# Kernel tuning notes

Hardware: AMD Instinct MI355X
Metric: run time of the kernel (lower is better)

The kernel has to match this reference:

```python
import jax, jax.numpy as jnp
import numpy as np

H = 32          # query heads
KVH = 8         # kv heads (GQA)
D = 128         # head dim
GROUP = 128     # quantization group size along K
THETA = 10000.0 # RoPE base


def dequant_fp4(codes, scales):
    """FP4 E2M1-style dequant: w = (code - 8) * 0.5 * per-group scale.
    codes: [K, N] int32 in [0,16); scales: [K//GROUP, N] float32."""
    K, N = codes.shape
    g = K // GROUP
    w = (codes.astype(jnp.float32) - 8.0) * 0.5
    return (w.reshape(g, GROUP, N) * scales[:, None, :]).reshape(K, N)


def apply_rope(x, pos):
    """x: [B, S, h, D]; rotate-half RoPE."""
    half = D // 2
    inv_freq = 1.0 / (THETA ** (jnp.arange(half, dtype=jnp.float32) / half))
    ang = pos.astype(jnp.float32)[:, None] * inv_freq[None, :]  # [S, half]
    cos = jnp.cos(ang)[None, :, None, :]
    sin = jnp.sin(ang)[None, :, None, :]
    x1, x2 = x[..., :half], x[..., half:]
    return jnp.concatenate([x1 * cos - x2 * sin, x2 * cos + x1 * sin], axis=-1)


def setup_inputs() -> dict:
    key = jax.random.key(0)
    ks = jax.random.split(key, 9)
    B, S, HID = 1, 2048, H * D
    KV = KVH * D
    x = jax.random.normal(ks[0], (B, S, HID), dtype=jnp.float32)
    q_codes = jax.random.randint(ks[1], (HID, HID), 0, 16, dtype=jnp.int32)
    k_codes = jax.random.randint(ks[2], (HID, KV), 0, 16, dtype=jnp.int32)
    v_codes = jax.random.randint(ks[3], (HID, KV), 0, 16, dtype=jnp.int32)
    o_codes = jax.random.randint(ks[4], (HID, HID), 0, 16, dtype=jnp.int32)
    g = HID // GROUP
    mk = lambda k, n: jax.random.uniform(k, (g, n), dtype=jnp.float32) * 0.02 + 1e-3
    q_scales = mk(ks[5], HID)
    k_scales = mk(ks[6], KV)
    v_scales = mk(ks[7], KV)
    o_scales = mk(ks[8], HID)
    return {"x": x, "q_codes": q_codes, "k_codes": k_codes, "v_codes": v_codes,
            "o_codes": o_codes, "q_scales": q_scales, "k_scales": k_scales,
            "v_scales": v_scales, "o_scales": o_scales}


def reference(x, q_codes, k_codes, v_codes, o_codes,
              q_scales, k_scales, v_scales, o_scales):
    B, S, _ = x.shape
    Wq = dequant_fp4(q_codes, q_scales)  # [HID, HID]
    Wk = dequant_fp4(k_codes, k_scales)  # [HID, KVH*D]
    Wv = dequant_fp4(v_codes, v_scales)
    Wo = dequant_fp4(o_codes, o_scales)

    q = (x @ Wq).reshape(B, S, H, D)
    k = (x @ Wk).reshape(B, S, KVH, D)
    v = (x @ Wv).reshape(B, S, KVH, D)

    pos = jnp.arange(S)
    q = apply_rope(q, pos)
    k = apply_rope(k, pos)

    # GQA: expand kv heads to query heads (this is what reading the shared
    # KV cache per query-head group computes)
    rep = H // KVH
    k = jnp.repeat(k, rep, axis=2)  # [B, S, H, D]
    v = jnp.repeat(v, rep, axis=2)

    scale = 1.0 / jnp.sqrt(jnp.float32(D))
    scores = jnp.einsum('bqhd,bkhd->bhqk', q, k) * scale  # [B, H, S, S]
    causal = jnp.tril(jnp.ones((S, S), dtype=bool))
    scores = jnp.where(causal[None, None], scores, jnp.float32(-1e30))
    probs = jax.nn.softmax(scores, axis=-1)
    attn = jnp.einsum('bhqk,bkhd->bqhd', probs, v).reshape(B, S, H * D)
    return attn @ Wo
```

## Files before the change

### kernel.cpp

```cpp
#include <hip/hip_runtime.h>

typedef unsigned short u16;
typedef __attribute__((ext_vector_type(4))) float f32x4;
typedef __attribute__((ext_vector_type(4))) unsigned short u16x4;
typedef __attribute__((ext_vector_type(8))) short bf16x8;

#define S_LEN 2048
#define NH 32
#define NKVH 8
#define DHEAD 128
#define HID 4096
#define KVW 1024
#define QKVW 6144

__device__ __forceinline__ u16 f2bf(float f) {
  unsigned u = __float_as_uint(f);
  u = u + 0x7fffu + ((u >> 16) & 1u);
  return (u16)(u >> 16);
}
__device__ __forceinline__ float bf2f(u16 h) {
  return __uint_as_float(((unsigned)h) << 16);
}
__device__ __forceinline__ void async16(void* lds, const void* g) {
  __builtin_amdgcn_global_load_lds((const __attribute__((address_space(1))) void*)g,
                                   (__attribute__((address_space(3))) void*)lds, 16, 0, 0);
}
__device__ __forceinline__ f32x4 mfma16(bf16x8 a, bf16x8 b, f32x4 c) {
  return __builtin_amdgcn_mfma_f32_16x16x32_bf16(a, b, c, 0, 0, 0);
}
__device__ __forceinline__ unsigned cvtpk(float a, float b) {
  unsigned r;
  asm("v_cvt_pk_bf16_f32 %0, %1, %2" : "=v"(r) : "v"(a), "v"(b));
  return r;
}

__global__ __launch_bounds__(256) void f2bf4_kernel(const float* __restrict__ in,
                                                    u16* __restrict__ out) {
  size_t i = ((size_t)blockIdx.x * 256 + threadIdx.x) * 4;
  f32x4 v = *(const f32x4*)(in + i);
  u16x4 o;
  o.x = f2bf(v.x); o.y = f2bf(v.y); o.z = f2bf(v.z); o.w = f2bf(v.w);
  *(u16x4*)(out + i) = o;
}

__global__ __launch_bounds__(256) void dequant_t_kernel(const int* __restrict__ codes,
                                                        const float* __restrict__ scales,
                                                        u16* __restrict__ Wt,
                                                        int K, int N) {
  __shared__ float tile[32][33];
  const int tx = threadIdx.x & 31, ty = threadIdx.x >> 5;
  const int k0 = blockIdx.x * 32, n0 = blockIdx.y * 32;
  const float sc = scales[(size_t)(k0 >> 7) * N + n0 + tx];
#pragma unroll
  for (int i = 0; i < 4; ++i) {
    int k = k0 + ty + i * 8;
    int c = codes[(size_t)k * N + n0 + tx];
    tile[ty + i * 8][tx] = ((float)c - 8.0f) * 0.5f * sc;
  }
  __syncthreads();
#pragma unroll
  for (int i = 0; i < 4; ++i) {
    int n = n0 + ty + i * 8;
    Wt[(size_t)n * K + k0 + tx] = f2bf(tile[tx][ty + i * 8]);
  }
}

template <int NI, int OUTF32>
__global__ __launch_bounds__(512, 2) void gemm_w(const u16* __restrict__ A, int lda,
                                                 const u16* __restrict__ Bt, int ldb,
                                                 void* __restrict__ Cv, int ldc, int K) {
  constexpr int BN = NI * 32;
  constexpr int NB = NI / 2;
  constexpr int BSLOT = BN * 128;
  extern __shared__ char lds[];
  char* Bbase = lds + 65536;
  const int tid = threadIdx.x, w = tid >> 6, lane = tid & 63;
  const int lo = lane & 15, hi = lane >> 4;
  const int wm = w >> 1, wn = w & 1;
  const int id = blockIdx.x;
  const int g = id & 7, r = id >> 3;
  const int bm = r >> 2, bn = g * 4 + (r & 3);
  const int m0 = bm * 256, n0 = bn * BN;

  const int srow = tid >> 3, schunk = (tid & 7) ^ (srow & 7);
  const char* Ab = (const char*)(A + (size_t)(m0 + srow) * lda) + schunk * 16;
  const char* Bb = (const char*)(Bt + (size_t)(n0 + srow) * ldb) + schunk * 16;

  f32x4 acc[4][NI];
#pragma unroll
  for (int i = 0; i < 4; ++i)
#pragma unroll
    for (int j = 0; j < NI; ++j) acc[i][j] = (f32x4){0.f, 0.f, 0.f, 0.f};

  auto stageA = [&](int buf, int k1) {
#pragma unroll
    for (int u = 0; u < 2; ++u) {
      char* dst = lds + buf * 32768 + u * 8192 + w * 1024;
      async16(dst, Ab + ((size_t)(u * 64) * lda + k1) * 2);
      async16(dst + 16384, Ab + ((size_t)(u * 64 + 128) * lda + k1) * 2);
    }
  };
  auto stageB = [&](int slot, int k1) {
#pragma unroll
    for (int j = 0; j < NB; ++j)
      async16(Bbase + slot * BSLOT + j * 8192 + w * 1024,
              Bb + ((size_t)(j * 64) * ldb + k1) * 2);
  };

  const int xm = (lo & 7) << 4;
  const int aro = (wm >> 1) * 16384 + (wm & 1) * 8192 + lo * 128;
  int bofs[NI];
#pragma unroll
  for (int ni = 0; ni < NI; ++ni) {
    int n = wn * (NI * 16) + ni * 16 + lo;
    bofs[ni] = (n >> 6) * 8192 + (n & 63) * 128;
  }

  auto ldfrags = [&](const char* As, const char* Bs, int kk, bf16x8* Afo, bf16x8* Bfo) {
    const int ck = (kk * 64 + hi * 16) ^ xm;
#pragma unroll
    for (int i = 0; i < 4; ++i) Afo[i] = *(const bf16x8*)(As + aro + i * 2048 + ck);
#pragma unroll
    for (int ni = 0; ni < NI; ++ni) Bfo[ni] = *(const bf16x8*)(Bs + bofs[ni] + ck);
  };

  stageA(0, 0);
  stageB(0, 0);
  stageB(1, 64);
  asm volatile("s_waitcnt vmcnt(%0)" ::"i"(NB) : "memory");
  __builtin_amdgcn_s_barrier();

  bf16x8 Afc[4], Bfc[NI], Afn[4], Bfn[NI];
  ldfrags(lds, Bbase, 0, Afc, Bfc);

  const int KT = K >> 6;
  int ab = 0, bb = 0;
  for (int t = 0; t < KT; ++t) {
    const char* As = lds + ab * 32768;
    const char* Bs = Bbase + bb * BSLOT;
    const bool m1 = t + 1 < KT, m2 = t + 2 < KT;
    int bs2 = bb + 2; if (bs2 >= 3) bs2 -= 3;
    int bn1 = bb + 1; if (bn1 >= 3) bn1 -= 3;
    if (m1) stageA(ab ^ 1, (t + 1) << 6);
    ldfrags(As, Bs, 1, Afn, Bfn);
    __builtin_amdgcn_sched_barrier(0);
    __builtin_amdgcn_s_setprio(1);
#pragma unroll
    for (int i = 0; i < 4; ++i)
#pragma unroll
      for (int ni = 0; ni < NI; ++ni)
        acc[i][ni] = mfma16(Afc[i], Bfc[ni], acc[i][ni]);
    __builtin_amdgcn_s_setprio(0);
    if (m2) stageB(bs2, (t + 2) << 6);
    __builtin_amdgcn_s_setprio(1);
#pragma unroll
    for (int i = 0; i < 4; ++i)
#pragma unroll
      for (int ni = 0; ni < NI; ++ni)
        acc[i][ni] = mfma16(Afn[i], Bfn[ni], acc[i][ni]);
    __builtin_amdgcn_s_setprio(0);
    if (m1) {
      if (m2) asm volatile("s_waitcnt vmcnt(%0)" ::"i"(NB) : "memory");
      else    asm volatile("s_waitcnt vmcnt(0)" ::: "memory");
      __builtin_amdgcn_s_barrier();
      ldfrags(lds + (ab ^ 1) * 32768, Bbase + bn1 * BSLOT, 0, Afc, Bfc);
      __builtin_amdgcn_sched_barrier(0);
    }
    ab ^= 1;
    if (++bb == 3) bb = 0;
  }
#pragma unroll
  for (int mi = 0; mi < 4; ++mi)
#pragma unroll
    for (int ni = 0; ni < NI; ++ni) {
      size_t row = (size_t)(m0 + wm * 64 + mi * 16 + hi * 4);
      size_t col = (size_t)(n0 + wn * (NI * 16) + ni * 16 + lo);
#pragma unroll
      for (int rr = 0; rr < 4; ++rr) {
        size_t idx = (row + rr) * ldc + col;
        if (OUTF32) ((float*)Cv)[idx] = acc[mi][ni][rr];
        else ((u16*)Cv)[idx] = f2bf(acc[mi][ni][rr]);
      }
    }
}

__global__ void rope_tab_kernel(float* __restrict__ ctab, float* __restrict__ stab) {
  int s = blockIdx.x, d = threadIdx.x;
  float inv = exp2f(-(float)d * 0.2076205059304601f);
  float ang = (float)s * inv;
  ctab[s * 64 + d] = cosf(ang);
  stab[s * 64 + d] = sinf(ang);
}

__global__ __launch_bounds__(256) void rope_kernel(u16* __restrict__ qkv,
                                                   const float* __restrict__ ctab,
                                                   const float* __restrict__ stab) {
  int s = blockIdx.x;
  int head = blockIdx.y * 4 + (threadIdx.x >> 6);
  int d = threadIdx.x & 63;
  int col = head < NH ? head * DHEAD + d : HID + (head - NH) * DHEAD + d;
  size_t base = (size_t)s * QKVW + col;
  float c = ctab[s * 64 + d], sn = stab[s * 64 + d];
  float x1 = bf2f(qkv[base]);
  float x2 = bf2f(qkv[base + 64]);
  qkv[base] = f2bf(x1 * c - x2 * sn);
  qkv[base + 64] = f2bf(x2 * c + x1 * sn);
}

__global__ __launch_bounds__(256) void vtrans_kernel(const u16* __restrict__ qkv,
                                                     u16* __restrict__ Vt) {
  __shared__ u16 tile[32][33];
  const int tx = threadIdx.x & 31, ty = threadIdx.x >> 5;
  const int s0 = blockIdx.x * 32, c0 = blockIdx.y * 32;
#pragma unroll
  for (int i = 0; i < 4; ++i)
    tile[ty + i * 8][tx] = qkv[(size_t)(s0 + ty + i * 8) * QKVW + (HID + KVW) + c0 + tx];
  __syncthreads();
#pragma unroll
  for (int i = 0; i < 4; ++i)
    Vt[(size_t)(c0 + ty + i * 8) * S_LEN + s0 + tx] = tile[tx][ty + i * 8];
}

__global__ __launch_bounds__(256) void attn_kernel(const u16* __restrict__ qkv,
                                                   const u16* __restrict__ Vt,
                                                   u16* __restrict__ attnO) {
  __shared__ alignas(16) u16 Ks[2][64 * 128];
  __shared__ alignas(16) u16 Vs[2][128 * 64];
  __shared__ alignas(16) unsigned Ps32[4][16][44];
  const int tid = threadIdx.x, w = tid >> 6, lane = tid & 63;
  const int lo = lane & 15, hi = lane >> 4;
  const int bx = blockIdx.x, h = blockIdx.y, kvh = h >> 2;
  const u16* Kbase = qkv + HID + kvh * DHEAD;
  const u16* Vbase = Vt + (size_t)kvh * DHEAD * S_LEN;
  const int krow = w * 4 + hi;
  const int kscn = lo;
  const int vrow = w * 8 + (lane >> 3);
  const int vscn = lane & 7;

#pragma unroll 1
  for (int pass = 0; pass < 2; ++pass) {
    const int qb = pass == 0 ? (31 - bx) : bx;
    const int qrow0 = qb * 64 + w * 16;
    bf16x8 qf[4];
    {
      const u16* qp = qkv + (size_t)(qrow0 + lo) * QKVW + h * DHEAD;
      const float qs = 0.08838834764831845f * 1.4426950408889634f;
#pragma unroll
      for (int dc = 0; dc < 4; ++dc) {
        bf16x8 v = *(const bf16x8*)(qp + dc * 32 + hi * 8);
#pragma unroll
        for (int j = 0; j < 8; ++j) v[j] = (short)f2bf(bf2f((u16)v[j]) * qs);
        qf[dc] = v;
      }
    }
    f32x4 oacc[8];
#pragma unroll
    for (int i = 0; i < 8; ++i) oacc[i] = (f32x4){0.f, 0.f, 0.f, 0.f};
    float m_run = -1e30f, l_run = 0.f;

    const int nt = qb + 1;
#pragma unroll
    for (int i = 0; i < 4; ++i) {
      int kr = i * 16 + krow;
      async16((char*)&Ks[0][0] + (i * 16 + w * 4) * 256,
              (const char*)(Kbase + (size_t)kr * QKVW + (kscn ^ (kr & 7)) * 8));
      int vr = i * 32 + vrow;
      async16((char*)&Vs[0][0] + (i * 32 + w * 8) * 128,
              (const char*)(Vbase + (size_t)vr * S_LEN + (vscn ^ (vr & 7)) * 8));
    }
    __syncthreads();
    for (int kt = 0; kt < nt; ++kt) {
      const int cur = kt & 1;
      if (kt + 1 < nt) {
#pragma unroll
        for (int i = 0; i < 4; ++i) {
          int kr = i * 16 + krow;
          async16((char*)&Ks[cur ^ 1][0] + (i * 16 + w * 4) * 256,
                  (const char*)(Kbase + (size_t)((kt + 1) * 64 + kr) * QKVW + (kscn ^ (kr & 7)) * 8));
          int vr = i * 32 + vrow;
          async16((char*)&Vs[cur ^ 1][0] + (i * 32 + w * 8) * 128,
                  (const char*)(Vbase + (size_t)vr * S_LEN + (kt + 1) * 64 + (vscn ^ (vr & 7)) * 8));
        }
      }
      f32x4 st[4];
#pragma unroll
      for (int t = 0; t < 4; ++t) st[t] = (f32x4){0.f, 0.f, 0.f, 0.f};
#pragma unroll
      for (int t = 0; t < 4; ++t) {
        int kq = t * 16 + lo;
#pragma unroll
        for (int dc = 0; dc < 4; ++dc) {
          bf16x8 kf = *(const bf16x8*)((const char*)&Ks[cur][0] + kq * 256 +
                                       (((dc << 2) + hi) ^ (kq & 7)) * 16);
          st[t] = mfma16(kf, qf[dc], st[t]);
        }
      }
      if (kt == qb) {
#pragma unroll
        for (int t = 0; t < 4; ++t)
#pragma unroll
          for (int r = 0; r < 4; ++r) {
            int kposl = t * 16 + 4 * hi + r;
            st[t][r] = (kposl <= w * 16 + lo) ? st[t][r] : -1e30f;
          }
      }
      float mloc = st[0][0];
#pragma unroll
      for (int t = 0; t < 4; ++t)
#pragma unroll
        for (int r = 0; r < 4; ++r) mloc = fmaxf(mloc, st[t][r]);
      mloc = fmaxf(mloc, __shfl_xor(mloc, 16, 64));
      mloc = fmaxf(mloc, __shfl_xor(mloc, 32, 64));
      if (!__all(mloc - m_run <= 8.0f)) {
        float mn = fmaxf(m_run, mloc);
        float alpha = exp2f(m_run - mn);
        m_run = mn;
        l_run *= alpha;
#pragma unroll
        for (int dt = 0; dt < 8; ++dt)
#pragma unroll
          for (int r = 0; r < 4; ++r) oacc[dt][r] *= alpha;
      }
      float psum = 0.f;
#pragma unroll
      for (int t = 0; t < 4; ++t)
#pragma unroll
        for (int r = 0; r < 4; ++r) {
          float p = exp2f(st[t][r] - m_run);
          st[t][r] = p;
          psum += p;
        }
      psum += __shfl_xor(psum, 16, 64);
      psum += __shfl_xor(psum, 32, 64);
      l_run += psum;
#pragma unroll
      for (int t = 0; t < 4; ++t)
#pragma unroll
        for (int rp = 0; rp < 2; ++rp)
          Ps32[w][lo][8 * t + 2 * hi + rp] = cvtpk(st[t][2 * rp], st[t][2 * rp + 1]);
      bf16x8 pf[2];
#pragma unroll
      for (int kc = 0; kc < 2; ++kc) pf[kc] = *(const bf16x8*)&Ps32[w][lo][kc * 16 + hi * 4];
#pragma unroll
      for (int dt = 0; dt < 8; ++dt) {
        int d = dt * 16 + lo;
#pragma unroll
        for (int kc = 0; kc < 2; ++kc) {
          bf16x8 vf = *(const bf16x8*)((const char*)&Vs[cur][0] + d * 128 +
                                       (((kc << 2) + hi) ^ (d & 7)) * 16);
          oacc[dt] = mfma16(vf, pf[kc], oacc[dt]);
        }
      }
      __syncthreads();
    }
    float linv = 1.0f / l_run;
    u16* op = attnO + (size_t)(qrow0 + lo) * HID + h * DHEAD;
#pragma unroll
    for (int dt = 0; dt < 8; ++dt) {
      u16x4 o4;
#pragma unroll
      for (int r = 0; r < 4; ++r) o4[r] = f2bf(oacc[dt][r] * linv);
      *(u16x4*)(op + dt * 16 + 4 * hi) = o4;
    }
  }
}

extern "C" void kernel_launch(void* const* d_in, const int* in_sizes, int n_in,
                              void* d_out, int out_size, void* d_ws, size_t ws_size,
                              hipStream_t stream) {
  const float* x = (const float*)d_in[0];
  const int* qc = (const int*)d_in[1];
  const int* kc = (const int*)d_in[2];
  const int* vc = (const int*)d_in[3];
  const int* oc = (const int*)d_in[4];
  const float* qs = (const float*)d_in[5];
  const float* ks = (const float*)d_in[6];
  const float* vs = (const float*)d_in[7];
  const float* os = (const float*)d_in[8];
  float* out = (float*)d_out;
  char* ws = (char*)d_ws;

  u16* xb    = (u16*)(ws);
  u16* qkv   = (u16*)(ws + 16777216);
  u16* attnb = (u16*)(ws + 41943040);
  u16* Vt    = (u16*)(ws + 58720256);
  u16* Wbig  = (u16*)(ws + 62914560);
  float* ctab = (float*)Vt;
  float* stab = (float*)(ws + 58720256 + 524288);

  f2bf4_kernel<<<8192, 256, 0, stream>>>(x, xb);
  dequant_t_kernel<<<dim3(128, 128), 256, 0, stream>>>(qc, qs, Wbig, HID, HID);
  dequant_t_kernel<<<dim3(128, 32), 256, 0, stream>>>(kc, ks, Wbig + (size_t)HID * HID, HID, KVW);
  dequant_t_kernel<<<dim3(128, 32), 256, 0, stream>>>(vc, vs, Wbig + (size_t)(HID + KVW) * HID, HID, KVW);
  rope_tab_kernel<<<2048, 64, 0, stream>>>(ctab, stab);
  gemm_w<6, 0><<<256, 512, 139264, stream>>>(xb, HID, Wbig, HID, qkv, QKVW, HID);
  rope_kernel<<<dim3(S_LEN, (NH + NKVH) / 4), 256, 0, stream>>>(qkv, ctab, stab);
  vtrans_kernel<<<dim3(64, 32), 256, 0, stream>>>(qkv, Vt);
  attn_kernel<<<dim3(16, 32), 256, 0, stream>>>(qkv, Vt, attnb);
  dequant_t_kernel<<<dim3(128, 128), 256, 0, stream>>>(oc, os, Wbig, HID, HID);
  gemm_w<4, 1><<<256, 512, 114688, stream>>>(attnb, HID, Wbig, HID, out, HID, HID);
}
```

Measured before the change: 322.7 us.

## Load K/V fragments directly from global into registers, drop LDS staging

```diff
diff --git a/kernel.cpp b/kernel.cpp
--- a/kernel.cpp
+++ b/kernel.cpp
@@ -221,21 +221,15 @@
     Vt[(size_t)(c0 + ty + i * 8) * S_LEN + s0 + tx] = tile[tx][ty + i * 8];
 }
 
-__global__ __launch_bounds__(256) void attn_kernel(const u16* __restrict__ qkv,
-                                                   const u16* __restrict__ Vt,
-                                                   u16* __restrict__ attnO) {
-  __shared__ alignas(16) u16 Ks[2][64 * 128];
-  __shared__ alignas(16) u16 Vs[2][128 * 64];
+__global__ __launch_bounds__(256, 3) void attn_kernel(const u16* __restrict__ qkv,
+                                                      const u16* __restrict__ Vt,
+                                                      u16* __restrict__ attnO) {
   __shared__ alignas(16) unsigned Ps32[4][16][44];
   const int tid = threadIdx.x, w = tid >> 6, lane = tid & 63;
   const int lo = lane & 15, hi = lane >> 4;
   const int bx = blockIdx.x, h = blockIdx.y, kvh = h >> 2;
-  const u16* Kbase = qkv + HID + kvh * DHEAD;
-  const u16* Vbase = Vt + (size_t)kvh * DHEAD * S_LEN;
-  const int krow = w * 4 + hi;
-  const int kscn = lo;
-  const int vrow = w * 8 + (lane >> 3);
-  const int vscn = lane & 7;
+  const u16* Kl = qkv + HID + kvh * DHEAD + (size_t)lo * QKVW + hi * 8;
+  const u16* Vl = Vt + (size_t)kvh * DHEAD * S_LEN + (size_t)lo * S_LEN + hi * 8;
 
 #pragma unroll 1
   for (int pass = 0; pass < 2; ++pass) {
@@ -259,42 +253,31 @@
     float m_run = -1e30f, l_run = 0.f;
 
     const int nt = qb + 1;
-#pragma unroll
-    for (int i = 0; i < 4; ++i) {
-      int kr = i * 16 + krow;
-      async16((char*)&Ks[0][0] + (i * 16 + w * 4) * 256,
-              (const char*)(Kbase + (size_t)kr * QKVW + (kscn ^ (kr & 7)) * 8));
-      int vr = i * 32 + vrow;
-      async16((char*)&Vs[0][0] + (i * 32 + w * 8) * 128,
-              (const char*)(Vbase + (size_t)vr * S_LEN + (vscn ^ (vr & 7)) * 8));
-    }
-    __syncthreads();
     for (int kt = 0; kt < nt; ++kt) {
-      const int cur = kt & 1;
-      if (kt + 1 < nt) {
-#pragma unroll
-        for (int i = 0; i < 4; ++i) {
-          int kr = i * 16 + krow;
-          async16((char*)&Ks[cur ^ 1][0] + (i * 16 + w * 4) * 256,
-                  (const char*)(Kbase + (size_t)((kt + 1) * 64 + kr) * QKVW + (kscn ^ (kr & 7)) * 8));
-          int vr = i * 32 + vrow;
-          async16((char*)&Vs[cur ^ 1][0] + (i * 32 + w * 8) * 128,
-                  (const char*)(Vbase + (size_t)vr * S_LEN + (kt + 1) * 64 + (vscn ^ (vr & 7)) * 8));
-        }
-      }
+      const u16* Kt_ = Kl + (size_t)(kt * 64) * QKVW;
+      const u16* Vc_ = Vl + kt * 64;
+      bf16x8 kf[4][4];
+#pragma unroll
+      for (int t = 0; t < 4; ++t)
+#pragma unroll
+        for (int dc = 0; dc < 4; ++dc)
+          kf[t][dc] = *(const bf16x8*)(Kt_ + (size_t)(t * 16) * QKVW + dc * 32);
       f32x4 st[4];
 #pragma unroll
       for (int t = 0; t < 4; ++t) st[t] = (f32x4){0.f, 0.f, 0.f, 0.f};
-#pragma unroll
-      for (int t = 0; t < 4; ++t) {
-        int kq = t * 16 + lo;
-#pragma unroll
-        for (int dc = 0; dc < 4; ++dc) {
-          bf16x8 kf = *(const bf16x8*)((const char*)&Ks[cur][0] + kq * 256 +
-                                       (((dc << 2) + hi) ^ (kq & 7)) * 16);
-          st[t] = mfma16(kf, qf[dc], st[t]);
-        }
-      }
+      __builtin_amdgcn_s_setprio(1);
+#pragma unroll
+      for (int dc = 0; dc < 4; ++dc)
+#pragma unroll
+        for (int t = 0; t < 4; ++t)
+          st[t] = mfma16(kf[t][dc], qf[dc], st[t]);
+      __builtin_amdgcn_s_setprio(0);
+      bf16x8 vf[8][2];
+#pragma unroll
+      for (int dt = 0; dt < 8; ++dt)
+#pragma unroll
+        for (int kc = 0; kc < 2; ++kc)
+          vf[dt][kc] = *(const bf16x8*)(Vc_ + (size_t)(dt * 16) * S_LEN + kc * 32);
       if (kt == qb) {
 #pragma unroll
         for (int t = 0; t < 4; ++t)
@@ -341,17 +324,13 @@
       bf16x8 pf[2];
 #pragma unroll
       for (int kc = 0; kc < 2; ++kc) pf[kc] = *(const bf16x8*)&Ps32[w][lo][kc * 16 + hi * 4];
-#pragma unroll
-      for (int dt = 0; dt < 8; ++dt) {
-        int d = dt * 16 + lo;
-#pragma unroll
-        for (int kc = 0; kc < 2; ++kc) {
-          bf16x8 vf = *(const bf16x8*)((const char*)&Vs[cur][0] + d * 128 +
-                                       (((kc << 2) + hi) ^ (d & 7)) * 16);
-          oacc[dt] = mfma16(vf, pf[kc], oacc[dt]);
-        }
-      }
-      __syncthreads();
+      __builtin_amdgcn_s_setprio(1);
+#pragma unroll
+      for (int dt = 0; dt < 8; ++dt)
+#pragma unroll
+        for (int kc = 0; kc < 2; ++kc)
+          oacc[dt] = mfma16(vf[dt][kc], pf[kc], oacc[dt]);
+      __builtin_amdgcn_s_setprio(0);
     }
     float linv = 1.0f / l_run;
     u16* op = attnO + (size_t)(qrow0 + lo) * HID + h * DHEAD;
```

After: 476.4 us. 1.48x slower.

## Split attention KV tile across wave pairs with 32-row query tiles and merge

Applied to the files above, without the earlier changes.

```diff
diff --git a/kernel.cpp b/kernel.cpp
--- a/kernel.cpp
+++ b/kernel.cpp
@@ -221,42 +221,48 @@
     Vt[(size_t)(c0 + ty + i * 8) * S_LEN + s0 + tx] = tile[tx][ty + i * 8];
 }
 
-__global__ __launch_bounds__(256) void attn_kernel(const u16* __restrict__ qkv,
-                                                   const u16* __restrict__ Vt,
-                                                   u16* __restrict__ attnO) {
+__global__ __launch_bounds__(256, 2) void attn_kernel(const u16* __restrict__ qkv,
+                                                      const u16* __restrict__ Vt,
+                                                      u16* __restrict__ attnO) {
   __shared__ alignas(16) u16 Ks[2][64 * 128];
   __shared__ alignas(16) u16 Vs[2][128 * 64];
-  __shared__ alignas(16) unsigned Ps32[4][16][44];
+  __shared__ alignas(16) unsigned Ps32[4][32][20];
   const int tid = threadIdx.x, w = tid >> 6, lane = tid & 63;
   const int lo = lane & 15, hi = lane >> 4;
-  const int bx = blockIdx.x, h = blockIdx.y, kvh = h >> 2;
+  const int p = w >> 1, h = w & 1;
+  const int bx = blockIdx.x, hd = blockIdx.y, kvh = hd >> 2;
   const u16* Kbase = qkv + HID + kvh * DHEAD;
   const u16* Vbase = Vt + (size_t)kvh * DHEAD * S_LEN;
   const int krow = w * 4 + hi;
   const int kscn = lo;
   const int vrow = w * 8 + (lane >> 3);
   const int vscn = lane & 7;
+  float* scrO = (p == 0) ? (float*)&Ks[0][0] : (float*)&Vs[0][0];
+  float* mls = (float*)&Ps32[0][0][0];
 
 #pragma unroll 1
   for (int pass = 0; pass < 2; ++pass) {
     const int qb = pass == 0 ? (31 - bx) : bx;
-    const int qrow0 = qb * 64 + w * 16;
-    bf16x8 qf[4];
-    {
-      const u16* qp = qkv + (size_t)(qrow0 + lo) * QKVW + h * DHEAD;
+    const int qrow0 = qb * 64 + p * 32;
+    bf16x8 qf[2][4];
+#pragma unroll
+    for (int nq = 0; nq < 2; ++nq) {
+      const u16* qp = qkv + (size_t)(qrow0 + nq * 16 + lo) * QKVW + hd * DHEAD;
       const float qs = 0.08838834764831845f * 1.4426950408889634f;
 #pragma unroll
       for (int dc = 0; dc < 4; ++dc) {
         bf16x8 v = *(const bf16x8*)(qp + dc * 32 + hi * 8);
 #pragma unroll
         for (int j = 0; j < 8; ++j) v[j] = (short)f2bf(bf2f((u16)v[j]) * qs);
-        qf[dc] = v;
-      }
-    }
-    f32x4 oacc[8];
-#pragma unroll
-    for (int i = 0; i < 8; ++i) oacc[i] = (f32x4){0.f, 0.f, 0.f, 0.f};
-    float m_run = -1e30f, l_run = 0.f;
+        qf[nq][dc] = v;
+      }
+    }
+    f32x4 oacc[8][2];
+#pragma unroll
+    for (int i = 0; i < 8; ++i)
+#pragma unroll
+      for (int nq = 0; nq < 2; ++nq) oacc[i][nq] = (f32x4){0.f, 0.f, 0.f, 0.f};
+    float m_run[2] = {-1e30f, -1e30f}, l_run[2] = {0.f, 0.f};
 
     const int nt = qb + 1;
 #pragma unroll
@@ -282,86 +288,148 @@
                   (const char*)(Vbase + (size_t)vr * S_LEN + (kt + 1) * 64 + (vscn ^ (vr & 7)) * 8));
         }
       }
-      f32x4 st[4];
-#pragma unroll
-      for (int t = 0; t < 4; ++t) st[t] = (f32x4){0.f, 0.f, 0.f, 0.f};
-#pragma unroll
-      for (int t = 0; t < 4; ++t) {
-        int kq = t * 16 + lo;
-#pragma unroll
-        for (int dc = 0; dc < 4; ++dc) {
-          bf16x8 kf = *(const bf16x8*)((const char*)&Ks[cur][0] + kq * 256 +
-                                       (((dc << 2) + hi) ^ (kq & 7)) * 16);
-          st[t] = mfma16(kf, qf[dc], st[t]);
-        }
+      const char* Kc = (const char*)&Ks[cur][0];
+      const char* Vc = (const char*)&Vs[cur][0];
+      bf16x8 kf[2][4];
+#pragma unroll
+      for (int t = 0; t < 2; ++t) {
+        const int kq = h * 32 + t * 16 + lo;
+#pragma unroll
+        for (int dc = 0; dc < 4; ++dc)
+          kf[t][dc] = *(const bf16x8*)(Kc + kq * 256 + ((((dc << 2) + hi)) ^ (kq & 7)) * 16);
+      }
+      f32x4 st[2][2];
+#pragma unroll
+      for (int nq = 0; nq < 2; ++nq)
+#pragma unroll
+        for (int t = 0; t < 2; ++t) st[nq][t] = (f32x4){0.f, 0.f, 0.f, 0.f};
+      __builtin_amdgcn_s_setprio(1);
+#pragma unroll
+      for (int dc = 0; dc < 4; ++dc)
+#pragma unroll
+        for (int nq = 0; nq < 2; ++nq)
+#pragma unroll
+          for (int t = 0; t < 2; ++t)
+            st[nq][t] = mfma16(kf[t][dc], qf[nq][dc], st[nq][t]);
+      __builtin_amdgcn_s_setprio(0);
+      bf16x8 vf[8];
+#pragma unroll
+      for (int dt = 0; dt < 8; ++dt) {
+        const int d = dt * 16 + lo;
+        vf[dt] = *(const bf16x8*)(Vc + d * 128 + (((h << 2) + hi) ^ (d & 7)) * 16);
       }
       if (kt == qb) {
 #pragma unroll
-        for (int t = 0; t < 4; ++t)
+        for (int nq = 0; nq < 2; ++nq)
+#pragma unroll
+          for (int t = 0; t < 2; ++t)
+#pragma unroll
+            for (int r = 0; r < 4; ++r) {
+              int kposl = h * 32 + t * 16 + 4 * hi + r;
+              st[nq][t][r] = (kposl <= p * 32 + nq * 16 + lo) ? st[nq][t][r] : -1e30f;
+            }
+      }
+#pragma unroll
+      for (int nq = 0; nq < 2; ++nq) {
+        float mloc = st[nq][0][0];
+#pragma unroll
+        for (int t = 0; t < 2; ++t)
+#pragma unroll
+          for (int r = 0; r < 4; ++r) mloc = fmaxf(mloc, st[nq][t][r]);
+        mloc = fmaxf(mloc, __shfl_xor(mloc, 16, 64));
+        mloc = fmaxf(mloc, __shfl_xor(mloc, 32, 64));
+        if (!__all(mloc - m_run[nq] <= 8.0f)) {
+          float mn = fmaxf(m_run[nq], mloc);
+          float alpha = exp2f(m_run[nq] - mn);
+          m_run[nq] = mn;
+          l_run[nq] *= alpha;
+#pragma unroll
+          for (int dt = 0; dt < 8; ++dt)
+#pragma unroll
+            for (int r = 0; r < 4; ++r) oacc[dt][nq][r] *= alpha;
+        }
+        float psum = 0.f;
+#pragma unroll
+        for (int t = 0; t < 2; ++t)
 #pragma unroll
           for (int r = 0; r < 4; ++r) {
-            int kposl = t * 16 + 4 * hi + r;
-            st[t][r] = (kposl <= w * 16 + lo) ? st[t][r] : -1e30f;
+            float pv = exp2f(st[nq][t][r] - m_run[nq]);
+            st[nq][t][r] = pv;
+            psum += pv;
           }
-      }
-      float mloc = st[0][0];
-#pragma unroll
-      for (int t = 0; t < 4; ++t)
-#pragma unroll
-        for (int r = 0; r < 4; ++r) mloc = fmaxf(mloc, st[t][r]);
-      mloc = fmaxf(mloc, __shfl_xor(mloc, 16, 64));
-      mloc = fmaxf(mloc, __shfl_xor(mloc, 32, 64));
-      if (!__all(mloc - m_run <= 8.0f)) {
-        float mn = fmaxf(m_run, mloc);
-        float alpha = exp2f(m_run - mn);
-        m_run = mn;
-        l_run *= alpha;
+        psum += __shfl_xor(psum, 16, 64);
+        psum += __shfl_xor(psum, 32, 64);
+        l_run[nq] += psum;
+#pragma unroll
+        for (int t = 0; t < 2; ++t) {
+          unsigned w0 = cvtpk(st[nq][t][0], st[nq][t][1]);
+          unsigned w1 = cvtpk(st[nq][t][2], st[nq][t][3]);
+          const int blk = (2 * t + (hi >> 1)) ^ (lo & 3);
+          unsigned* dst = &Ps32[w][nq * 16 + lo][blk * 4 + 2 * (hi & 1)];
+          dst[0] = w0;
+          dst[1] = w1;
+        }
+      }
+      bf16x8 pf[2];
+#pragma unroll
+      for (int nq = 0; nq < 2; ++nq)
+        pf[nq] = *(const bf16x8*)&Ps32[w][nq * 16 + lo][(hi ^ (lo & 3)) << 2];
+      __builtin_amdgcn_s_setprio(1);
+#pragma unroll
+      for (int dt = 0; dt < 8; ++dt)
+#pragma unroll
+        for (int nq = 0; nq < 2; ++nq)
+          oacc[dt][nq] = mfma16(vf[dt], pf[nq], oacc[dt][nq]);
+      __builtin_amdgcn_s_setprio(0);
+      __syncthreads();
+    }
+    if (h == 1) {
+#pragma unroll
+      for (int nq = 0; nq < 2; ++nq) {
+        if (hi == 0) {
+          mls[p * 64 + nq * 16 + lo] = m_run[nq];
+          mls[128 + p * 64 + nq * 16 + lo] = l_run[nq];
+        }
 #pragma unroll
         for (int dt = 0; dt < 8; ++dt)
-#pragma unroll
-          for (int r = 0; r < 4; ++r) oacc[dt][r] *= alpha;
-      }
-      float psum = 0.f;
-#pragma unroll
-      for (int t = 0; t < 4; ++t)
-#pragma unroll
-        for (int r = 0; r < 4; ++r) {
-          float p = exp2f(st[t][r] - m_run);
-          st[t][r] = p;
-          psum += p;
-        }
-      psum += __shfl_xor(psum, 16, 64);
-      psum += __shfl_xor(psum, 32, 64);
-      l_run += psum;
-#pragma unroll
-      for (int t = 0; t < 4; ++t)
-#pragma unroll
-        for (int rp = 0; rp < 2; ++rp)
-          Ps32[w][lo][8 * t + 2 * hi + rp] = cvtpk(st[t][2 * rp], st[t][2 * rp + 1]);
-      bf16x8 pf[2];
-#pragma unroll
-      for (int kc = 0; kc < 2; ++kc) pf[kc] = *(const bf16x8*)&Ps32[w][lo][kc * 16 + hi * 4];
-#pragma unroll
-      for (int dt = 0; dt < 8; ++dt) {
-        int d = dt * 16 + lo;
-#pragma unroll
-        for (int kc = 0; kc < 2; ++kc) {
-          bf16x8 vf = *(const bf16x8*)((const char*)&Vs[cur][0] + d * 128 +
-                                       (((kc << 2) + hi) ^ (d & 7)) * 16);
-          oacc[dt] = mfma16(vf, pf[kc], oacc[dt]);
-        }
-      }
-      __syncthreads();
-    }
-    float linv = 1.0f / l_run;
-    u16* op = attnO + (size_t)(qrow0 + lo) * HID + h * DHEAD;
-#pragma unroll
-    for (int dt = 0; dt < 8; ++dt) {
-      u16x4 o4;
-#pragma unroll
-      for (int r = 0; r < 4; ++r) o4[r] = f2bf(oacc[dt][r] * linv);
-      *(u16x4*)(op + dt * 16 + 4 * hi) = o4;
-    }
+          *(f32x4*)&scrO[(nq * 16 + lo) * 132 + dt * 16 + 4 * hi] = oacc[dt][nq];
+      }
+    }
+    __syncthreads();
+    if (h == 0) {
+      float aa[2], ab[2];
+#pragma unroll
+      for (int nq = 0; nq < 2; ++nq) {
+        float m_b = mls[p * 64 + nq * 16 + lo];
+        float l_b = mls[128 + p * 64 + nq * 16 + lo];
+        float mm = fmaxf(m_run[nq], m_b);
+        aa[nq] = exp2f(m_run[nq] - mm);
+        ab[nq] = exp2f(m_b - mm);
+        l_run[nq] = l_run[nq] * aa[nq] + l_b * ab[nq];
+      }
+#pragma unroll
+      for (int dt = 0; dt < 8; ++dt)
+#pragma unroll
+        for (int nq = 0; nq < 2; ++nq) {
+          f32x4 ob = *(const f32x4*)&scrO[(nq * 16 + lo) * 132 + dt * 16 + 4 * hi];
+#pragma unroll
+          for (int r = 0; r < 4; ++r)
+            oacc[dt][nq][r] = oacc[dt][nq][r] * aa[nq] + ob[r] * ab[nq];
+        }
+#pragma unroll
+      for (int nq = 0; nq < 2; ++nq) {
+        float linv = 1.0f / l_run[nq];
+        u16* op = attnO + (size_t)(qrow0 + nq * 16 + lo) * HID + hd * DHEAD;
+#pragma unroll
+        for (int dt = 0; dt < 8; ++dt) {
+          u16x4 o4;
+#pragma unroll
+          for (int r = 0; r < 4; ++r) o4[r] = f2bf(oacc[dt][nq][r] * linv);
+          *(u16x4*)(op + dt * 16 + 4 * hi) = o4;
+        }
+      }
+    }
+    __syncthreads();
   }
 }
 
```

Measured after the change: 324.9 us. Within noise of the previous version (+0.7%).

## Rewrite attention with 32x32 MFMA tiles, 128-row query blocks, and permlane P exchange

Applied to the files above, without the earlier changes.

```diff
diff --git a/kernel.cpp b/kernel.cpp
--- a/kernel.cpp
+++ b/kernel.cpp
@@ -2,7 +2,10 @@
 
 typedef unsigned short u16;
 typedef __attribute__((ext_vector_type(4))) float f32x4;
+typedef __attribute__((ext_vector_type(16))) float f32x16;
 typedef __attribute__((ext_vector_type(4))) unsigned short u16x4;
+typedef __attribute__((ext_vector_type(4))) unsigned u32x4;
+typedef __attribute__((ext_vector_type(2))) unsigned u32x2;
 typedef __attribute__((ext_vector_type(8))) short bf16x8;
 
 #define S_LEN 2048
@@ -28,10 +31,16 @@
 __device__ __forceinline__ f32x4 mfma16(bf16x8 a, bf16x8 b, f32x4 c) {
   return __builtin_amdgcn_mfma_f32_16x16x32_bf16(a, b, c, 0, 0, 0);
 }
+__device__ __forceinline__ f32x16 mfma32(bf16x8 a, bf16x8 b, f32x16 c) {
+  return __builtin_amdgcn_mfma_f32_32x32x16_bf16(a, b, c, 0, 0, 0);
+}
 __device__ __forceinline__ unsigned cvtpk(float a, float b) {
   unsigned r;
   asm("v_cvt_pk_bf16_f32 %0, %1, %2" : "=v"(r) : "v"(a), "v"(b));
   return r;
+}
+__device__ __forceinline__ u32x2 pl32(unsigned a, unsigned b) {
+  return __builtin_amdgcn_permlane32_swap(a, b, 0, 0);
 }
 
 __global__ __launch_bounds__(256) void f2bf4_kernel(const float* __restrict__ in,
@@ -221,148 +230,165 @@
     Vt[(size_t)(c0 + ty + i * 8) * S_LEN + s0 + tx] = tile[tx][ty + i * 8];
 }
 
-__global__ __launch_bounds__(256) void attn_kernel(const u16* __restrict__ qkv,
-                                                   const u16* __restrict__ Vt,
-                                                   u16* __restrict__ attnO) {
+__global__ __launch_bounds__(256, 2) void attn_kernel(const u16* __restrict__ qkv,
+                                                      const u16* __restrict__ Vt,
+                                                      u16* __restrict__ attnO) {
   __shared__ alignas(16) u16 Ks[2][64 * 128];
   __shared__ alignas(16) u16 Vs[2][128 * 64];
-  __shared__ alignas(16) unsigned Ps32[4][16][44];
   const int tid = threadIdx.x, w = tid >> 6, lane = tid & 63;
-  const int lo = lane & 15, hi = lane >> 4;
-  const int bx = blockIdx.x, h = blockIdx.y, kvh = h >> 2;
+  const int l31 = lane & 31, hi5 = lane >> 5;
+  const int bx = blockIdx.x, hd = blockIdx.y, kvh = hd >> 2;
+  const int qb = (hd < 16) ? (15 - bx) : bx;
+  const int qrow0 = qb * 128 + w * 32;
+  const int qg = qrow0 + l31;
   const u16* Kbase = qkv + HID + kvh * DHEAD;
   const u16* Vbase = Vt + (size_t)kvh * DHEAD * S_LEN;
-  const int krow = w * 4 + hi;
-  const int kscn = lo;
-  const int vrow = w * 8 + (lane >> 3);
-  const int vscn = lane & 7;
-
-#pragma unroll 1
-  for (int pass = 0; pass < 2; ++pass) {
-    const int qb = pass == 0 ? (31 - bx) : bx;
-    const int qrow0 = qb * 64 + w * 16;
-    bf16x8 qf[4];
-    {
-      const u16* qp = qkv + (size_t)(qrow0 + lo) * QKVW + h * DHEAD;
-      const float qs = 0.08838834764831845f * 1.4426950408889634f;
-#pragma unroll
-      for (int dc = 0; dc < 4; ++dc) {
-        bf16x8 v = *(const bf16x8*)(qp + dc * 32 + hi * 8);
-#pragma unroll
-        for (int j = 0; j < 8; ++j) v[j] = (short)f2bf(bf2f((u16)v[j]) * qs);
-        qf[dc] = v;
-      }
-    }
-    f32x4 oacc[8];
-#pragma unroll
-    for (int i = 0; i < 8; ++i) oacc[i] = (f32x4){0.f, 0.f, 0.f, 0.f};
-    float m_run = -1e30f, l_run = 0.f;
-
-    const int nt = qb + 1;
+  const int krow = w * 4 + (lane >> 4), kscn = lane & 15;
+  const int vrow = w * 8 + (lane >> 3), vscn = lane & 7;
+
+  auto stage = [&](int buf, int kt) {
 #pragma unroll
     for (int i = 0; i < 4; ++i) {
       int kr = i * 16 + krow;
-      async16((char*)&Ks[0][0] + (i * 16 + w * 4) * 256,
-              (const char*)(Kbase + (size_t)kr * QKVW + (kscn ^ (kr & 7)) * 8));
+      async16((char*)&Ks[buf][0] + (i * 16 + w * 4) * 256,
+              (const char*)(Kbase + (size_t)(kt * 64 + kr) * QKVW + (kscn ^ (kr & 7)) * 8));
       int vr = i * 32 + vrow;
-      async16((char*)&Vs[0][0] + (i * 32 + w * 8) * 128,
-              (const char*)(Vbase + (size_t)vr * S_LEN + (vscn ^ (vr & 7)) * 8));
-    }
-    __syncthreads();
-    for (int kt = 0; kt < nt; ++kt) {
-      const int cur = kt & 1;
-      if (kt + 1 < nt) {
-#pragma unroll
-        for (int i = 0; i < 4; ++i) {
-          int kr = i * 16 + krow;
-          async16((char*)&Ks[cur ^ 1][0] + (i * 16 + w * 4) * 256,
-                  (const char*)(Kbase + (size_t)((kt + 1) * 64 + kr) * QKVW + (kscn ^ (kr & 7)) * 8));
-          int vr = i * 32 + vrow;
-          async16((char*)&Vs[cur ^ 1][0] + (i * 32 + w * 8) * 128,
-                  (const char*)(Vbase + (size_t)vr * S_LEN + (kt + 1) * 64 + (vscn ^ (vr & 7)) * 8));
-        }
-      }
-      f32x4 st[4];
-#pragma unroll
-      for (int t = 0; t < 4; ++t) st[t] = (f32x4){0.f, 0.f, 0.f, 0.f};
-#pragma unroll
-      for (int t = 0; t < 4; ++t) {
-        int kq = t * 16 + lo;
-#pragma unroll
-        for (int dc = 0; dc < 4; ++dc) {
-          bf16x8 kf = *(const bf16x8*)((const char*)&Ks[cur][0] + kq * 256 +
-                                       (((dc << 2) + hi) ^ (kq & 7)) * 16);
-          st[t] = mfma16(kf, qf[dc], st[t]);
-        }
-      }
-      if (kt == qb) {
-#pragma unroll
-        for (int t = 0; t < 4; ++t)
-#pragma unroll
-          for (int r = 0; r < 4; ++r) {
-            int kposl = t * 16 + 4 * hi + r;
-            st[t][r] = (kposl <= w * 16 + lo) ? st[t][r] : -1e30f;
+      async16((char*)&Vs[buf][0] + (i * 32 + w * 8) * 128,
+              (const char*)(Vbase + (size_t)vr * S_LEN + kt * 64 + (vscn ^ (vr & 7)) * 8));
+    }
+  };
+
+  bf16x8 qf[8];
+  {
+    const u16* qp = qkv + (size_t)qg * QKVW + hd * DHEAD + hi5 * 8;
+    const float qs = 0.08838834764831845f * 1.4426950408889634f;
+#pragma unroll
+    for (int dsl = 0; dsl < 8; ++dsl) {
+      bf16x8 v = *(const bf16x8*)(qp + dsl * 16);
+#pragma unroll
+      for (int j = 0; j < 8; ++j) v[j] = (short)f2bf(bf2f((u16)v[j]) * qs);
+      qf[dsl] = v;
+    }
+  }
+  f32x16 oacc[4];
+#pragma unroll
+  for (int db = 0; db < 4; ++db)
+#pragma unroll
+    for (int r = 0; r < 16; ++r) oacc[db][r] = 0.f;
+  float m_run = -1e30f, l_run = 0.f;
+
+  const int nt = 2 * (qb + 1);
+  stage(0, 0);
+  __syncthreads();
+  for (int kt = 0; kt < nt; ++kt) {
+    const int cur = kt & 1;
+    if (kt + 1 < nt) stage(cur ^ 1, kt + 1);
+    if (kt * 64 <= qrow0 + 31) {
+      const char* Kc = (const char*)&Ks[cur][0];
+      const char* Vc = (const char*)&Vs[cur][0];
+      bf16x8 kf0[8], kf1[8];
+#pragma unroll
+      for (int dsl = 0; dsl < 8; ++dsl) {
+        kf0[dsl] = *(const bf16x8*)(Kc + l31 * 256 + ((2 * dsl + hi5) ^ (l31 & 7)) * 16);
+        kf1[dsl] = *(const bf16x8*)(Kc + (32 + l31) * 256 +
+                                    ((2 * dsl + hi5) ^ ((32 + l31) & 7)) * 16);
+      }
+      f32x16 st[2];
+#pragma unroll
+      for (int r = 0; r < 16; ++r) { st[0][r] = 0.f; st[1][r] = 0.f; }
+      __builtin_amdgcn_s_setprio(1);
+#pragma unroll
+      for (int dsl = 0; dsl < 8; ++dsl) {
+        st[0] = mfma32(kf0[dsl], qf[dsl], st[0]);
+        st[1] = mfma32(kf1[dsl], qf[dsl], st[1]);
+      }
+      __builtin_amdgcn_s_setprio(0);
+      if (kt >= 2 * qb) {
+#pragma unroll
+        for (int blk = 0; blk < 2; ++blk)
+#pragma unroll
+          for (int r = 0; r < 16; ++r) {
+            int kpg = kt * 64 + blk * 32 + (r & 3) + 8 * (r >> 2) + 4 * hi5;
+            st[blk][r] = (kpg <= qg) ? st[blk][r] : -1e30f;
           }
       }
-      float mloc = st[0][0];
-#pragma unroll
-      for (int t = 0; t < 4; ++t)
-#pragma unroll
-        for (int r = 0; r < 4; ++r) mloc = fmaxf(mloc, st[t][r]);
-      mloc = fmaxf(mloc, __shfl_xor(mloc, 16, 64));
-      mloc = fmaxf(mloc, __shfl_xor(mloc, 32, 64));
+      float tm[16];
+#pragma unroll
+      for (int r = 0; r < 16; ++r) tm[r] = fmaxf(st[0][r], st[1][r]);
+#pragma unroll
+      for (int off = 8; off >= 1; off >>= 1)
+#pragma unroll
+        for (int r = 0; r < off; ++r) tm[r] = fmaxf(tm[r], tm[r + off]);
+      float mloc;
+      {
+        u32x2 rr = pl32(__float_as_uint(tm[0]), __float_as_uint(tm[0]));
+        mloc = fmaxf(__uint_as_float(rr.x), __uint_as_float(rr.y));
+      }
       if (!__all(mloc - m_run <= 8.0f)) {
         float mn = fmaxf(m_run, mloc);
         float alpha = exp2f(m_run - mn);
         m_run = mn;
         l_run *= alpha;
 #pragma unroll
-        for (int dt = 0; dt < 8; ++dt)
-#pragma unroll
-          for (int r = 0; r < 4; ++r) oacc[dt][r] *= alpha;
-      }
-      float psum = 0.f;
-#pragma unroll
-      for (int t = 0; t < 4; ++t)
-#pragma unroll
-        for (int r = 0; r < 4; ++r) {
-          float p = exp2f(st[t][r] - m_run);
-          st[t][r] = p;
-          psum += p;
+        for (int db = 0; db < 4; ++db)
+#pragma unroll
+          for (int r = 0; r < 16; ++r) oacc[db][r] *= alpha;
+      }
+#pragma unroll
+      for (int blk = 0; blk < 2; ++blk)
+#pragma unroll
+        for (int r = 0; r < 16; ++r) st[blk][r] = exp2f(st[blk][r] - m_run);
+      float ts[16];
+#pragma unroll
+      for (int r = 0; r < 16; ++r) ts[r] = st[0][r] + st[1][r];
+#pragma unroll
+      for (int off = 8; off >= 1; off >>= 1)
+#pragma unroll
+        for (int r = 0; r < off; ++r) ts[r] += ts[r + off];
+      {
+        u32x2 rr = pl32(__float_as_uint(ts[0]), __float_as_uint(ts[0]));
+        l_run += __uint_as_float(rr.x) + __uint_as_float(rr.y);
+      }
+      bf16x8 pf[4];
+#pragma unroll
+      for (int s = 0; s < 4; ++s) {
+        const int blk = s >> 1, r0 = (s & 1) * 8;
+        unsigned a0 = cvtpk(st[blk][r0 + 0], st[blk][r0 + 1]);
+        unsigned a1 = cvtpk(st[blk][r0 + 2], st[blk][r0 + 3]);
+        unsigned b0 = cvtpk(st[blk][r0 + 4], st[blk][r0 + 5]);
+        unsigned b1 = cvtpk(st[blk][r0 + 6], st[blk][r0 + 7]);
+        u32x2 r0p = pl32(a0, b0);
+        u32x2 r1p = pl32(a1, b1);
+        u32x4 t; t.x = r0p.x; t.y = r1p.x; t.z = r0p.y; t.w = r1p.y;
+        pf[s] = __builtin_bit_cast(bf16x8, t);
+      }
+      __builtin_amdgcn_s_setprio(1);
+#pragma unroll
+      for (int s = 0; s < 4; ++s) {
+        bf16x8 vf[4];
+#pragma unroll
+        for (int db = 0; db < 4; ++db) {
+          const int row = db * 32 + l31;
+          vf[db] = *(const bf16x8*)(Vc + row * 128 + ((2 * s + hi5) ^ (row & 7)) * 16);
         }
-      psum += __shfl_xor(psum, 16, 64);
-      psum += __shfl_xor(psum, 32, 64);
-      l_run += psum;
-#pragma unroll
-      for (int t = 0; t < 4; ++t)
-#pragma unroll
-        for (int rp = 0; rp < 2; ++rp)
-          Ps32[w][lo][8 * t + 2 * hi + rp] = cvtpk(st[t][2 * rp], st[t][2 * rp + 1]);
-      bf16x8 pf[2];
-#pragma unroll
-      for (int kc = 0; kc < 2; ++kc) pf[kc] = *(const bf16x8*)&Ps32[w][lo][kc * 16 + hi * 4];
-#pragma unroll
-      for (int dt = 0; dt < 8; ++dt) {
-        int d = dt * 16 + lo;
-#pragma unroll
-        for (int kc = 0; kc < 2; ++kc) {
-          bf16x8 vf = *(const bf16x8*)((const char*)&Vs[cur][0] + d * 128 +
-                                       (((kc << 2) + hi) ^ (d & 7)) * 16);
-          oacc[dt] = mfma16(vf, pf[kc], oacc[dt]);
-        }
-      }
-      __syncthreads();
-    }
-    float linv = 1.0f / l_run;
-    u16* op = attnO + (size_t)(qrow0 + lo) * HID + h * DHEAD;
-#pragma unroll
-    for (int dt = 0; dt < 8; ++dt) {
+#pragma unroll
+        for (int db = 0; db < 4; ++db) oacc[db] = mfma32(vf[db], pf[s], oacc[db]);
+      }
+      __builtin_amdgcn_s_setprio(0);
+    }
+    __syncthreads();
+  }
+  float linv = 1.0f / l_run;
+  u16* op = attnO + (size_t)qg * HID + hd * DHEAD;
+#pragma unroll
+  for (int db = 0; db < 4; ++db)
+#pragma unroll
+    for (int g = 0; g < 4; ++g) {
       u16x4 o4;
 #pragma unroll
-      for (int r = 0; r < 4; ++r) o4[r] = f2bf(oacc[dt][r] * linv);
-      *(u16x4*)(op + dt * 16 + 4 * hi) = o4;
-    }
-  }
+      for (int r2 = 0; r2 < 4; ++r2) o4[r2] = f2bf(oacc[db][g * 4 + r2] * linv);
+      *(u16x4*)(op + db * 32 + 8 * g + 4 * hi5) = o4;
+    }
 }
 
 extern "C" void kernel_launch(void* const* d_in, const int* in_sizes, int n_in,
```

Result: no change. 323.5 us (+0.2%).
